# Performance work log

Measured on AMD Instinct MI355X. Metric: run time of the kernel, lower is better.

The kernel has to match this reference:

```python
import jax, jax.numpy as jnp
import numpy as np

TAPS = 5
DELAY = 3
ITERATIONS = 2
EPS = 1e-10


def wpe_one_iteration(Y, power, taps=TAPS, delay=DELAY, eps=EPS):
    """One WPE iteration.
    Y: (B, F, C, T) complex STFT signal.
    power: (B, F, T) real power estimate.
    Returns dereverberated signal, same shape as Y.
    """
    B, F, C, T = Y.shape
    inv_pow = 1.0 / jnp.maximum(power, eps)  # (B,F,T)

    # Tap-delayed (Toeplitz-like) stacked signal: Ytil[..., p, d, t] = Y[..., d, t - delay - p]
    Ytil = jnp.stack(
        [jnp.pad(Y[..., : T - delay - p], ((0, 0), (0, 0), (0, 0), (delay + p, 0)))
         for p in range(taps)],
        axis=2,
    )  # (B, F, taps, C, T)

    # Original implementation only accumulates statistics for frames where the
    # full tap window is available: t >= delay + taps - 1.
    valid = (jnp.arange(T) >= delay + taps - 1).astype(power.dtype)
    w = inv_pow * valid  # (B,F,T)

    Psi_w = jnp.conj(Ytil) * w[:, :, None, None, :]  # (B,F,taps,C,T)

    # Power-weighted covariance matrix R[(p,d),(q,e)] and cross-correlation b[(p,d),e]
    R = jnp.einsum('bfpdt,bfqet->bfpdqe', Psi_w, Ytil).reshape(B, F, taps * C, taps * C)
    b = jnp.einsum('bfpdt,bfet->bfpde', Psi_w, Y).reshape(B, F, taps * C, C)

    eye = jnp.eye(taps * C, dtype=R.dtype)
    # Batched per-frequency linear solve for the conjugate filter matrix
    G_conj = jnp.linalg.solve(R + eps * eye, b).reshape(B, F, taps, C, C)

    # reverb tail: sum over taps p and source channels d
    reverb_tail = jnp.einsum('bfpde,bfpdt->bfet', G_conj, Ytil)
    return Y - reverb_tail


def setup_inputs() -> dict:
    key = jax.random.key(0)
    k1, k2 = jax.random.split(key)
    B, T, C, F = 8, 512, 8, 257
    data_real = jax.random.normal(k1, (B, T, C, F), dtype=jnp.float32)
    data_imag = jax.random.normal(k2, (B, T, C, F), dtype=jnp.float32)
    ilens = jnp.full((B,), T, dtype=jnp.int64)
    return {"data_real": data_real, "data_imag": data_imag, "ilens": ilens}


def reference(data_real, data_imag, ilens):
    # data: (B, T, C, F) -> (B, F, C, T)
    data = (data_real + 1j * data_imag).astype(jnp.complex64)
    Y = jnp.transpose(data, (0, 3, 2, 1))  # (B,F,C,T)
    enhanced = Y
    for _ in range(ITERATIONS):
        power = jnp.mean(enhanced.real ** 2 + enhanced.imag ** 2, axis=-2)  # (B,F,T)
        enhanced = wpe_one_iteration(Y, power)
        # NOTE: original code calls `enhanced.masked_fill(...)` (non in-place),
        # whose result is discarded -> it is a no-op; ilens here are all == T anyway.
    enhanced = jnp.transpose(enhanced, (0, 3, 2, 1))  # (B,T,C,F)
    # Return real/imag stacked so output is a real float tensor (B,T,C,F,2)
    return jnp.stack([enhanced.real, enhanced.imag], axis=-1)
```

## Files before the change

kernel.cpp:

```cpp
#include <hip/hip_runtime.h>

constexpr int BB = 8;
constexpr int TT = 512;
constexpr int CHN = 8;
constexpr int FF = 257;
constexpr int TAPS = 5;
constexpr int DELAY = 3;
constexpr int NBF = BB * FF;
constexpr int ROWQ = 20;
constexpr int MC = 48;
constexpr int RS = 98;
constexpr int PROWS = 264;

typedef short s8v __attribute__((ext_vector_type(8)));
typedef float f4  __attribute__((ext_vector_type(4)));
typedef float v2f __attribute__((ext_vector_type(2)));
#define FMA2(a, b, c) __builtin_elementwise_fma((a), (b), (c))

__global__ void k_pack(const float* __restrict__ re, const float* __restrict__ im,
                       float* __restrict__ Yg, float* __restrict__ pw) {
  const int ft = blockIdx.x, tt = blockIdx.y, b = blockIdx.z;
  const int f0 = ft * 32, t0 = tt * 16;
  __shared__ float ls[32 * 258];
  const int tid = threadIdx.x;
  const int l = tid & 31;
  const int r = tid >> 5;
  const int f = f0 + l;
  if (f < FF) {
    for (int k = 0; k < 32; ++k) {
      const int task = r + 8 * k;
      const int ri = task & 1;
      const int c  = (task >> 1) & 7;
      const int t  = task >> 4;
      const float* src = ri ? im : re;
      const float v = src[(((size_t)b * TT + t0 + t) * CHN + c) * FF + f];
      ls[l * 258 + (t * 16 + c * 2 + ri)] = v;
    }
  }
  __syncthreads();
  for (int ff = 0; ff < 32; ++ff) {
    const int fg = f0 + ff;
    if (fg >= FF) break;
    Yg[(((size_t)b * FF + fg) * TT + t0) * 16 + tid] = ls[ff * 258 + tid];
  }
  if (f < FF) {
#pragma unroll
    for (int s = 0; s < 2; ++s) {
      const int t = (tid >> 5) + 8 * s;
      const float* row = &ls[l * 258 + t * 16];
      float ss = 0.f;
#pragma unroll
      for (int q = 0; q < 8; ++q) {
        const float2 v = *(const float2*)&row[q * 2];
        ss += v.x * v.x + v.y * v.y;
      }
      pw[((size_t)b * FF + f) * TT + t0 + t] = ss * (1.0f / CHN);
    }
  }
}

__device__ __forceinline__ unsigned bf16rn(float x) {
  unsigned b = __float_as_uint(x);
  return (b + 0x7fffu + ((b >> 16) & 1u)) >> 16;
}

__global__ __launch_bounds__(384, 4)
void k_corr(const float* __restrict__ Yg,
            const float* __restrict__ pw,
            float2* __restrict__ Mg) {
  const int bf = blockIdx.x;
  __shared__ float pre[PROWS * 9];
  __shared__ float pim[PROWS * 9];
  __shared__ unsigned short tiles[4 * 1920];
  const int tid = threadIdx.x;

  const int lane = tid & 63, wv = tid >> 6;
  const int rt = (wv < 3) ? 0 : (wv < 5 ? 1 : 2);
  const int ct = (wv < 3) ? wv : (wv < 5 ? wv - 2 : 2);
  const int lr = lane & 15, lk = lane >> 4;
  const int aoff = (rt * 16 + lr) * 40 + lk * 8;
  const int boff = (ct * 16 + lr) * 40 + lk * 8;

  f4 accre  = {0.f, 0.f, 0.f, 0.f};
  f4 accim1 = {0.f, 0.f, 0.f, 0.f};
  f4 accim2 = {0.f, 0.f, 0.f, 0.f};

  const float4* ybase4 = (const float4*)(Yg + (size_t)bf * TT * 16);

  for (int ch = 0; ch < 2; ++ch) {
    const int t0c = ch * 256;
    const int r0  = (ch == 0) ? 0 : (t0c - 7);
    const int nr  = 256 + (t0c - r0);
    for (int fi = tid; fi < nr * 4; fi += 384) {
      const int row = fi >> 2, q = fi & 3;
      const float4 v = ybase4[(size_t)(r0 + row) * 4 + q];
      pre[row * 9 + 2 * q] = v.x; pre[row * 9 + 2 * q + 1] = v.z;
      pim[row * 9 + 2 * q] = v.y; pim[row * 9 + 2 * q + 1] = v.w;
    }
    for (int t = t0c + tid; t < t0c + 256; t += 384) {
      const float p = pw[(size_t)bf * TT + t];
      pre[(t - r0) * 9 + 8] =
          (t >= DELAY + TAPS - 1) ? rsqrtf(fmaxf(p, 1e-10f)) : 0.0f;
    }
    __syncthreads();

    for (int ktl = 0; ktl < 8; ++ktl) {
      const int kt0 = t0c + ktl * 32;
#pragma unroll
      for (int cc = 0; cc < 2; ++cc) {
        const int c = tid + cc * 384;
        const int kp = c & 15, row = c >> 4;
        const int t = kt0 + 2 * kp;
        const int sh = (row < 40) ? (DELAY + (row >> 3)) : 0;
        const int e  = (row < 40) ? (row & 7) : (row - 40);
        int s0 = t - sh;     if (s0 < 0) s0 = 0;
        int s1 = t + 1 - sh; if (s1 < 0) s1 = 0;
        const float u0 = pre[(t - r0) * 9 + 8], u1 = pre[(t + 1 - r0) * 9 + 8];
        const float v0r = u0 * pre[(s0 - r0) * 9 + e];
        const float v0i = u0 * pim[(s0 - r0) * 9 + e];
        const float v1r = u1 * pre[(s1 - r0) * 9 + e];
        const float v1i = u1 * pim[(s1 - r0) * 9 + e];
        const int idx = row * 40 + 2 * kp;
        {
          const unsigned b0 = __float_as_uint(v0r), b1 = __float_as_uint(v1r);
          *(unsigned*)&tiles[idx] = (b0 >> 16) | (b1 & 0xffff0000u);
          *(unsigned*)&tiles[1920 + idx] =
              bf16rn(v0r - __uint_as_float(b0 & 0xffff0000u)) |
              (bf16rn(v1r - __uint_as_float(b1 & 0xffff0000u)) << 16);
        }
        {
          const unsigned b0 = __float_as_uint(v0i), b1 = __float_as_uint(v1i);
          *(unsigned*)&tiles[3840 + idx] = (b0 >> 16) | (b1 & 0xffff0000u);
          *(unsigned*)&tiles[5760 + idx] =
              bf16rn(v0i - __uint_as_float(b0 & 0xffff0000u)) |
              (bf16rn(v1i - __uint_as_float(b1 & 0xffff0000u)) << 16);
        }
      }
      __syncthreads();
      const s8v crhA = *(const s8v*)&tiles[aoff];
      const s8v crlA = *(const s8v*)&tiles[1920 + aoff];
      const s8v cihA = *(const s8v*)&tiles[3840 + aoff];
      const s8v cilA = *(const s8v*)&tiles[5760 + aoff];
      const s8v crhB = *(const s8v*)&tiles[boff];
      const s8v crlB = *(const s8v*)&tiles[1920 + boff];
      const s8v cihB = *(const s8v*)&tiles[3840 + boff];
      const s8v cilB = *(const s8v*)&tiles[5760 + boff];
      accre  = __builtin_amdgcn_mfma_f32_16x16x32_bf16(crhA, crhB, accre, 0, 0, 0);
      accre  = __builtin_amdgcn_mfma_f32_16x16x32_bf16(crlA, crhB, accre, 0, 0, 0);
      accre  = __builtin_amdgcn_mfma_f32_16x16x32_bf16(crhA, crlB, accre, 0, 0, 0);
      accre  = __builtin_amdgcn_mfma_f32_16x16x32_bf16(cihA, cihB, accre, 0, 0, 0);
      accre  = __builtin_amdgcn_mfma_f32_16x16x32_bf16(cilA, cihB, accre, 0, 0, 0);
      accre  = __builtin_amdgcn_mfma_f32_16x16x32_bf16(cihA, cilB, accre, 0, 0, 0);
      accim1 = __builtin_amdgcn_mfma_f32_16x16x32_bf16(crhA, cihB, accim1, 0, 0, 0);
      accim1 = __builtin_amdgcn_mfma_f32_16x16x32_bf16(crlA, cihB, accim1, 0, 0, 0);
      accim1 = __builtin_amdgcn_mfma_f32_16x16x32_bf16(crhA, cilB, accim1, 0, 0, 0);
      accim2 = __builtin_amdgcn_mfma_f32_16x16x32_bf16(cihA, crhB, accim2, 0, 0, 0);
      accim2 = __builtin_amdgcn_mfma_f32_16x16x32_bf16(cilA, crhB, accim2, 0, 0, 0);
      accim2 = __builtin_amdgcn_mfma_f32_16x16x32_bf16(cihA, crlB, accim2, 0, 0, 0);
      __syncthreads();
    }
  }

#pragma unroll
  for (int r = 0; r < 4; ++r) {
    const int i = rt * 16 + lk * 4 + r;
    const int j = ct * 16 + lr;
    const float revl = accre[r];
    const float imvl = accim1[r] - accim2[r];
    if (i < 40) {
      float rr = revl;
      if (i == j) rr += 1e-10f;
      Mg[((size_t)bf * 40 + i) * MC + j] = make_float2(rr, imvl);
    }
    if (rt < ct && j < 40) {
      Mg[((size_t)bf * 40 + j) * MC + i] = make_float2(revl, -imvl);
    }
  }
}

__global__ __launch_bounds__(128) void k_solve(const float2* __restrict__ Mg,
                                               float2* __restrict__ Gg) {
  const int bf = blockIdx.x;
  __shared__ float ml[40 * RS];
  const int tid = threadIdx.x;
  for (int idx = tid; idx < 40 * MC; idx += 128) {
    const int i = idx / MC, j = idx - i * MC;
    float2 v = Mg[((size_t)bf * 40 + i) * MC + j];
    *(float2*)&ml[i * RS + j * 2] = v;
  }
  __syncthreads();
  const int li = tid >> 3, lj = tid & 7;
  for (int k = 0; k < 40; ++k) {
    const float inr = __builtin_amdgcn_rcpf(ml[k * RS + k * 2]);
    for (int i = k + 1 + li; i < 40; i += 16) {
      const float2 aik = *(float2*)&ml[i * RS + k * 2];
      const float fr = aik.x * inr;
      const float fi = aik.y * inr;
      for (int j = k + 1 + lj; j < MC; j += 8) {
        const float2 ak = *(float2*)&ml[k * RS + j * 2];
        float2 ai = *(float2*)&ml[i * RS + j * 2];
        ai.x -= fr * ak.x - fi * ak.y;
        ai.y -= fr * ak.y + fi * ak.x;
        *(float2*)&ml[i * RS + j * 2] = ai;
      }
    }
    __syncthreads();
  }
  const int lane = tid & 63, wave = tid >> 6;
  const int e = 4 * wave + (lane & 3), cc = lane >> 2;
  for (int k = 39; k >= 0; --k) {
    float sr = 0.f, si = 0.f;
    for (int j = k + 1 + cc; j < 40; j += 16) {
      const float2 u = *(float2*)&ml[k * RS + j * 2];
      const float2 x = *(float2*)&ml[j * RS + (40 + e) * 2];
      sr += u.x * x.x - u.y * x.y;
      si += u.x * x.y + u.y * x.x;
    }
    sr += __shfl_xor(sr, 4);  si += __shfl_xor(si, 4);
    sr += __shfl_xor(sr, 8);  si += __shfl_xor(si, 8);
    sr += __shfl_xor(sr, 16); si += __shfl_xor(si, 16);
    sr += __shfl_xor(sr, 32); si += __shfl_xor(si, 32);
    if (cc == 0) {
      const float inr = __builtin_amdgcn_rcpf(ml[k * RS + k * 2]);
      const float2 rhs = *(float2*)&ml[k * RS + (40 + e) * 2];
      *(float2*)&ml[k * RS + (40 + e) * 2] =
          make_float2((rhs.x - sr) * inr, (rhs.y - si) * inr);
    }
    asm volatile("" ::: "memory");
  }
  __syncthreads();
  for (int idx = tid; idx < 320; idx += 128) {
    const int i = idx >> 3, ee = idx & 7;
    Gg[(size_t)bf * 320 + idx] = *(float2*)&ml[i * RS + (40 + ee) * 2];
  }
}

template <int MODE>
__global__ __launch_bounds__(256) void k_tail(float* __restrict__ Yg,
                                              const float2* __restrict__ Gg,
                                              float* __restrict__ pw) {
  const int bf = blockIdx.x;
  __shared__ float yl[TT * ROWQ];
  __shared__ float gl[640];
  const int tid = threadIdx.x;
  for (int idx = tid; idx < 320; idx += 256) {
    float2 g = Gg[(size_t)bf * 320 + idx];
    *(float2*)&gl[idx * 2] = make_float2(-g.x, -g.y);
  }
  const float4* ybase4 = (const float4*)(Yg + (size_t)bf * TT * 16);
  for (int fi = tid; fi < TT * 4; fi += 256) {
    const int row = fi >> 2, wq = fi & 3;
    *((float4*)&yl[row * ROWQ + wq * 4]) = ybase4[fi];
  }
  __syncthreads();

  const int t0 = tid;
  const int t1 = tid + 256;
  v2f acc[2][8];
  {
    const float* yr0 = &yl[t0 * ROWQ];
    const float* yr1 = &yl[t1 * ROWQ];
#pragma unroll
    for (int q = 0; q < 8; ++q) {
      const float2 a = *(const float2*)&yr0[2 * q];
      const float2 b = *(const float2*)&yr1[2 * q];
      acc[0][q] = (v2f){a.x, a.y};
      acc[1][q] = (v2f){b.x, b.y};
    }
  }
#pragma unroll 1
  for (int p = 0; p < TAPS; ++p) {
    const int rp0 = t0 - DELAY - p;
    const int rp1 = t1 - DELAY - p;
    const float* yrow0 = &yl[(rp0 >= 0 ? rp0 : 0) * ROWQ];
    const float* yrow1 = &yl[rp1 * ROWQ];
    const float m0 = (rp0 >= 0) ? 1.0f : 0.0f;
    const float* gp = &gl[p * 128];
#pragma unroll
    for (int d = 0; d < CHN; ++d) {
      const float2 y0 = *(const float2*)&yrow0[2 * d];
      const float2 y1 = *(const float2*)&yrow1[2 * d];
      const float y0r = m0 * y0.x, y0i = m0 * y0.y;
      const v2f yv0 = (v2f){y0r, y0i},  ys0 = (v2f){-y0i, y0r};
      const v2f yv1 = (v2f){y1.x, y1.y}, ys1 = (v2f){-y1.y, y1.x};
      const float4 g0 = *(const float4*)&gp[d * 16 + 0];
      const float4 g1 = *(const float4*)&gp[d * 16 + 4];
      const float4 g2 = *(const float4*)&gp[d * 16 + 8];
      const float4 g3 = *(const float4*)&gp[d * 16 + 12];
      const float ngr[8] = {g0.x, g0.z, g1.x, g1.z, g2.x, g2.z, g3.x, g3.z};
      const float ngi[8] = {g0.y, g0.w, g1.y, g1.w, g2.y, g2.w, g3.y, g3.w};
#pragma unroll
      for (int ee = 0; ee < 8; ++ee) {
        const v2f r2 = (v2f){ngr[ee], ngr[ee]};
        const v2f i2 = (v2f){ngi[ee], ngi[ee]};
        acc[0][ee] = FMA2(r2, yv0, FMA2(i2, ys0, acc[0][ee]));
        acc[1][ee] = FMA2(r2, yv1, FMA2(i2, ys1, acc[1][ee]));
      }
    }
  }
  float* ybase = Yg + (size_t)bf * TT * 16;
  if (MODE == 0) {
#pragma unroll
    for (int s = 0; s < 2; ++s) {
      const int t = tid + s * 256;
      float ss = 0.f;
#pragma unroll
      for (int q = 0; q < 8; ++q)
        ss += acc[s][q].x * acc[s][q].x + acc[s][q].y * acc[s][q].y;
      pw[(size_t)bf * TT + t] = ss * (1.0f / CHN);
    }
  } else {
#pragma unroll
    for (int s = 0; s < 2; ++s) {
      const int t = tid + s * 256;
      float4* dst = (float4*)(ybase + (size_t)t * 16);
#pragma unroll
      for (int q = 0; q < 4; ++q)
        dst[q] = make_float4(acc[s][2 * q].x, acc[s][2 * q].y,
                             acc[s][2 * q + 1].x, acc[s][2 * q + 1].y);
    }
  }
}

__global__ void k_unpack(const float* __restrict__ Yg, float* __restrict__ out) {
  const int ft = blockIdx.x, tt = blockIdx.y, b = blockIdx.z;
  const int f0 = ft * 32, t0 = tt * 16;
  __shared__ float ls[32 * 258];
  const int tid = threadIdx.x;
  for (int ff = 0; ff < 32; ++ff) {
    const int fg = f0 + ff;
    if (fg >= FF) break;
    ls[ff * 258 + tid] = Yg[(((size_t)b * FF + fg) * TT + t0) * 16 + tid];
  }
  __syncthreads();
  const int l = tid & 31, r = tid >> 5;
  const int fg = f0 + l;
  if (fg < FF) {
    for (int k = 0; k < 16; ++k) {
      const int task = r + 8 * k;
      const int t = task >> 3, c = task & 7;
      const float2 v = *(float2*)&ls[l * 258 + t * 16 + c * 2];
      *(float2*)&out[((((size_t)b * TT + t0 + t) * CHN + c) * FF + fg) * 2] = v;
    }
  }
}

extern "C" void kernel_launch(void* const* d_in, const int* in_sizes, int n_in,
                              void* d_out, int out_size, void* d_ws, size_t ws_size,
                              hipStream_t stream) {
  const float* re = (const float*)d_in[0];
  const float* im = (const float*)d_in[1];
  float* ws = (float*)d_ws;

  float*  Yg = ws;
  float*  pw = Yg + (size_t)NBF * TT * 16;
  float2* Mg = (float2*)(pw + (size_t)NBF * TT);
  float2* Gg = Mg + (size_t)NBF * 40 * MC;
  float*  out = (float*)d_out;

  const dim3 gridT(9, 32, BB);
  k_pack<<<gridT, 256, 0, stream>>>(re, im, Yg, pw);

  for (int iter = 0; iter < 2; ++iter) {
    k_corr<<<NBF, 384, 0, stream>>>(Yg, pw, Mg);
    k_solve<<<NBF, 128, 0, stream>>>(Mg, Gg);
    if (iter == 0)
      k_tail<0><<<NBF, 256, 0, stream>>>(Yg, Gg, pw);
    else
      k_tail<1><<<NBF, 256, 0, stream>>>(Yg, Gg, pw);
  }

  k_unpack<<<gridT, 256, 0, stream>>>(Yg, out);
}
```

Baseline: 424.8 us.

## Process reverb-tail time axis in two halo chunks to shrink LDS footprint

```diff
diff --git a/kernel.cpp b/kernel.cpp
--- a/kernel.cpp
+++ b/kernel.cpp
@@ -11,6 +11,7 @@
 constexpr int MC = 48;
 constexpr int RS = 98;
 constexpr int PROWS = 264;
+constexpr int TROWS = 263;
 
 typedef short s8v __attribute__((ext_vector_type(8)));
 typedef float f4  __attribute__((ext_vector_type(4)));
@@ -240,7 +241,7 @@
                                               const float2* __restrict__ Gg,
                                               float* __restrict__ pw) {
   const int bf = blockIdx.x;
-  __shared__ float yl[TT * ROWQ];
+  __shared__ float yl[TROWS * ROWQ];
   __shared__ float gl[640];
   const int tid = threadIdx.x;
   for (int idx = tid; idx < 320; idx += 256) {
@@ -248,76 +249,67 @@
     *(float2*)&gl[idx * 2] = make_float2(-g.x, -g.y);
   }
   const float4* ybase4 = (const float4*)(Yg + (size_t)bf * TT * 16);
-  for (int fi = tid; fi < TT * 4; fi += 256) {
-    const int row = fi >> 2, wq = fi & 3;
-    *((float4*)&yl[row * ROWQ + wq * 4]) = ybase4[fi];
-  }
-  __syncthreads();
-
-  const int t0 = tid;
-  const int t1 = tid + 256;
-  v2f acc[2][8];
-  {
-    const float* yr0 = &yl[t0 * ROWQ];
-    const float* yr1 = &yl[t1 * ROWQ];
-#pragma unroll
-    for (int q = 0; q < 8; ++q) {
-      const float2 a = *(const float2*)&yr0[2 * q];
-      const float2 b = *(const float2*)&yr1[2 * q];
-      acc[0][q] = (v2f){a.x, a.y};
-      acc[1][q] = (v2f){b.x, b.y};
-    }
-  }
+  float* ybase = Yg + (size_t)bf * TT * 16;
+
+  for (int ch = 1; ch >= 0; --ch) {
+    const int t0c = ch * 256;
+    const int r0  = (ch == 0) ? 0 : (t0c - 7);
+    const int nr  = 256 + (t0c - r0);
+    __syncthreads();
+    for (int fi = tid; fi < nr * 4; fi += 256) {
+      const int row = fi >> 2, wq = fi & 3;
+      *((float4*)&yl[row * ROWQ + wq * 4]) = ybase4[(size_t)(r0 + row) * 4 + wq];
+    }
+    __syncthreads();
+
+    const int t = t0c + tid;
+    const int lt = t - r0;
+    v2f acc[8];
+    {
+      const float* yr = &yl[lt * ROWQ];
+#pragma unroll
+      for (int q = 0; q < 8; ++q) {
+        const float2 a = *(const float2*)&yr[2 * q];
+        acc[q] = (v2f){a.x, a.y};
+      }
+    }
 #pragma unroll 1
-  for (int p = 0; p < TAPS; ++p) {
-    const int rp0 = t0 - DELAY - p;
-    const int rp1 = t1 - DELAY - p;
-    const float* yrow0 = &yl[(rp0 >= 0 ? rp0 : 0) * ROWQ];
-    const float* yrow1 = &yl[rp1 * ROWQ];
-    const float m0 = (rp0 >= 0) ? 1.0f : 0.0f;
-    const float* gp = &gl[p * 128];
-#pragma unroll
-    for (int d = 0; d < CHN; ++d) {
-      const float2 y0 = *(const float2*)&yrow0[2 * d];
-      const float2 y1 = *(const float2*)&yrow1[2 * d];
-      const float y0r = m0 * y0.x, y0i = m0 * y0.y;
-      const v2f yv0 = (v2f){y0r, y0i},  ys0 = (v2f){-y0i, y0r};
-      const v2f yv1 = (v2f){y1.x, y1.y}, ys1 = (v2f){-y1.y, y1.x};
-      const float4 g0 = *(const float4*)&gp[d * 16 + 0];
-      const float4 g1 = *(const float4*)&gp[d * 16 + 4];
-      const float4 g2 = *(const float4*)&gp[d * 16 + 8];
-      const float4 g3 = *(const float4*)&gp[d * 16 + 12];
-      const float ngr[8] = {g0.x, g0.z, g1.x, g1.z, g2.x, g2.z, g3.x, g3.z};
-      const float ngi[8] = {g0.y, g0.w, g1.y, g1.w, g2.y, g2.w, g3.y, g3.w};
-#pragma unroll
-      for (int ee = 0; ee < 8; ++ee) {
-        const v2f r2 = (v2f){ngr[ee], ngr[ee]};
-        const v2f i2 = (v2f){ngi[ee], ngi[ee]};
-        acc[0][ee] = FMA2(r2, yv0, FMA2(i2, ys0, acc[0][ee]));
-        acc[1][ee] = FMA2(r2, yv1, FMA2(i2, ys1, acc[1][ee]));
-      }
-    }
-  }
-  float* ybase = Yg + (size_t)bf * TT * 16;
-  if (MODE == 0) {
-#pragma unroll
-    for (int s = 0; s < 2; ++s) {
-      const int t = tid + s * 256;
+    for (int p = 0; p < TAPS; ++p) {
+      const int rp = t - DELAY - p;
+      const float* yrow = &yl[((rp >= 0 ? rp : 0) - (rp >= 0 ? r0 : 0)) * ROWQ];
+      const float m = (rp >= 0) ? 1.0f : 0.0f;
+      const float* gp = &gl[p * 128];
+#pragma unroll
+      for (int d = 0; d < CHN; ++d) {
+        const float2 y = *(const float2*)&yrow[2 * d];
+        const float yr = m * y.x, yi = m * y.y;
+        const v2f yv = (v2f){yr, yi}, ys = (v2f){-yi, yr};
+        const float4 g0 = *(const float4*)&gp[d * 16 + 0];
+        const float4 g1 = *(const float4*)&gp[d * 16 + 4];
+        const float4 g2 = *(const float4*)&gp[d * 16 + 8];
+        const float4 g3 = *(const float4*)&gp[d * 16 + 12];
+        const float ngr[8] = {g0.x, g0.z, g1.x, g1.z, g2.x, g2.z, g3.x, g3.z};
+        const float ngi[8] = {g0.y, g0.w, g1.y, g1.w, g2.y, g2.w, g3.y, g3.w};
+#pragma unroll
+        for (int ee = 0; ee < 8; ++ee) {
+          const v2f r2 = (v2f){ngr[ee], ngr[ee]};
+          const v2f i2 = (v2f){ngi[ee], ngi[ee]};
+          acc[ee] = FMA2(r2, yv, FMA2(i2, ys, acc[ee]));
+        }
+      }
+    }
+    if (MODE == 0) {
       float ss = 0.f;
 #pragma unroll
       for (int q = 0; q < 8; ++q)
-        ss += acc[s][q].x * acc[s][q].x + acc[s][q].y * acc[s][q].y;
+        ss += acc[q].x * acc[q].x + acc[q].y * acc[q].y;
       pw[(size_t)bf * TT + t] = ss * (1.0f / CHN);
-    }
-  } else {
-#pragma unroll
-    for (int s = 0; s < 2; ++s) {
-      const int t = tid + s * 256;
+    } else {
       float4* dst = (float4*)(ybase + (size_t)t * 16);
 #pragma unroll
       for (int q = 0; q < 4; ++q)
-        dst[q] = make_float4(acc[s][2 * q].x, acc[s][2 * q].y,
-                             acc[s][2 * q + 1].x, acc[s][2 * q + 1].y);
+        dst[q] = make_float4(acc[2 * q].x, acc[2 * q].y,
+                             acc[2 * q + 1].x, acc[2 * q + 1].y);
     }
   }
 }
```

Measured after the change: 418.6 us (median of 2 runs). Within noise of the previous version (-1.4%).
